# Optimization experiments

Measured on AMD Instinct MI355X. Metric: run time of the kernel, lower is better.

## Reference

```python
import jax, jax.numpy as jnp
import numpy as np
from jax import lax
import math

S, V, D, L, B = 64, 50257, 586, 4, 32  # seq_len, num_tokens, num_inputs, num_layers, batch_size
K1 = S // 4 + 1   # 17, conv1 kernel
P1 = S // 16 + 1  # 5,  avgpool1 kernel
P2 = S // 32 + 1  # 3,  avgpool2 kernel
EPS = 1e-5


def setup_inputs() -> dict:
    key = jax.random.key(0)
    ks = jax.random.split(key, 14)
    tokens = jax.random.randint(ks[0], (S, B), 0, V)
    emb = jax.random.normal(ks[1], (V, D - 3), jnp.float32) * 0.02
    # pos_embeds = randn(S,1,3).repeat(1,B,1)
    pos = jnp.tile(jax.random.normal(ks[2], (S, 1, 3), jnp.float32), (1, B, 1))
    gamma = 1.0 + 0.1 * jax.random.normal(ks[3], (L, S), jnp.float32)
    beta = 0.1 * jax.random.normal(ks[4], (L, S), jnp.float32)
    w1 = jax.random.normal(ks[5], (B // 2, B, K1), jnp.float32) * 0.02
    b1 = jax.random.normal(ks[6], (B // 2,), jnp.float32) * 0.02
    w2 = jax.random.normal(ks[7], (B // 4, B // 2, 1), jnp.float32) * 0.02
    b2 = jax.random.normal(ks[8], (B // 4,), jnp.float32) * 0.02
    w3 = jax.random.normal(ks[9], (B, B // 4, 3), jnp.float32) * 0.02
    b3 = jax.random.normal(ks[10], (B,), jnp.float32) * 0.02
    wl = jax.random.normal(ks[11], (128, 36), jnp.float32) * 0.1
    bl = jax.random.normal(ks[12], (128,), jnp.float32) * 0.1
    return {"tokens": tokens, "emb": emb, "pos": pos, "gamma": gamma, "beta": beta,
            "w1": w1, "b1": b1, "w2": w2, "b2": b2, "w3": w3, "b3": b3,
            "wl": wl, "bl": bl}


def _conv1d(x, w, b):
    # x: (N, C_in, Lx), w: (C_out, C_in, K)
    y = lax.conv_general_dilated(x, w, (1,), 'VALID',
                                 dimension_numbers=('NCH', 'OIH', 'NCH'))
    return y + b[None, :, None]


def _avgpool1d(x, k):
    # torch AvgPool1d: stride=kernel, floor mode
    n, c, lx = x.shape
    lo = lx // k
    return x[:, :, :lo * k].reshape(n, c, lo, k).mean(axis=-1)


def _logits(tokens, emb, pos, gamma, beta, w1, b1, w2, b2, w3, b3, wl, bl):
    x = emb[tokens] * math.sqrt(D)          # (S, B, D-3)
    x = jnp.concatenate([x, pos], axis=2)   # (S, B, D)
    for l in range(L):
        xb = x.swapaxes(0, 1)               # (B, S, D): BatchNorm1d over channels=S
        mean = xb.mean(axis=(0, 2), keepdims=True)
        var = xb.var(axis=(0, 2), keepdims=True)  # biased, training-mode batch stats
        xb = gamma[l][None, :, None] * (xb - mean) * lax.rsqrt(var + EPS) + beta[l][None, :, None]
        x = xb.swapaxes(0, 1)
    out = _conv1d(x, w1, b1)                # (S, B/2, D-16) = (64, 16, 570)
    out = _avgpool1d(out, P1)               # (64, 16, 114)
    out = _conv1d(out, w2, b2)              # (64, 8, 114)
    out = _avgpool1d(out, P2)               # (64, 8, 38)
    out = _conv1d(out, w3, b3)              # (64, 32, 36)
    out = jnp.einsum('sbk,vk->sbv', out, wl) + bl  # (64, 32, 128)
    return out


def reference(tokens, emb, pos, gamma, beta, w1, b1, w2, b2, w3, b3, wl, bl):
    out = _logits(tokens, emb, pos, gamma, beta, w1, b1, w2, b2, w3, b3, wl, bl)
    # vectorized replacement for the triple-nested .item() argmax loop
    return jnp.argmax(out, axis=-1).astype(jnp.float32)  # (S, B)
```

## Files before the change

kernel.cpp:

```cpp
#include <hip/hip_runtime.h>
#include <math.h>

#define SS 64
#define BB 32
#define DD 586
#define DE 583
#define U1 114
#define U2 38
#define T3 36
#define NTOK 18752

__global__ __launch_bounds__(256) void k_stats(
    const int* __restrict__ tokens, const float* __restrict__ emb,
    const float* __restrict__ pos, const float* __restrict__ gamma,
    const float* __restrict__ beta, float* __restrict__ alpha,
    float* __restrict__ delta)
{
  const int s = blockIdx.x;
  const int tid = threadIdx.x;
  const float sqrtD = 24.207436873820409f;
  __shared__ int stok[BB];
  if (tid < BB) stok[tid] = tokens[s*BB + tid];
  __syncthreads();
  double sum = 0.0, sq = 0.0;
  for (int idx = tid; idx < BB*DE; idx += 256) {
    int b = idx / DE;
    int d = idx - b*DE;
    float v = emb[(size_t)stok[b]*DE + d] * sqrtD;
    sum += v; sq += (double)v * v;
  }
  if (tid < BB*3) {
    float v = pos[s*BB*3 + tid];
    sum += v; sq += (double)v * v;
  }
  for (int off = 32; off > 0; off >>= 1) {
    sum += __shfl_down(sum, off);
    sq  += __shfl_down(sq, off);
  }
  __shared__ double rs_[4], rq_[4];
  int wid = tid >> 6;
  if ((tid & 63) == 0) { rs_[wid] = sum; rq_[wid] = sq; }
  __syncthreads();
  if (tid == 0) {
    double St = rs_[0]+rs_[1]+rs_[2]+rs_[3];
    double Qt = rq_[0]+rq_[1]+rq_[2]+rq_[3];
    double m0d = St / (double)NTOK;
    float m0 = (float)m0d;
    float v0 = (float)(Qt / (double)NTOK - m0d*m0d);
    float a = 1.0f;
    for (int l = 0; l < 4; ++l) {
      float rs = 1.0f / sqrtf(a*a*v0 + 1e-5f);
      a = gamma[l*SS + s] * rs * a;
    }
    alpha[s] = a;
    delta[s] = beta[3*SS + s] - a * m0;
  }
}

__global__ __launch_bounds__(256) void k_conv1(
    const int* __restrict__ tokens, const float* __restrict__ emb,
    const float* __restrict__ pos, const float* __restrict__ w1,
    const float* __restrict__ alpha, const float* __restrict__ delta,
    float* __restrict__ part)
{
  const int s = blockIdx.x;
  const int g = blockIdx.y;
  const int tid = threadIdx.x;
  const float sqrtD = 24.207436873820409f;
  __shared__ float xs[8*587];
  __shared__ __align__(16) float wp[8*21*16];
  __shared__ int stok[8];
  if (tid < 8) stok[tid] = tokens[s*BB + g*8 + tid];
  __syncthreads();
  const float al = alpha[s], de = delta[s];
  for (int idx = tid; idx < 8*DD; idx += 256) {
    int cc = idx / DD;
    int d = idx - cc*DD;
    float v;
    if (d < DE) v = emb[(size_t)stok[cc]*DE + d] * sqrtD;
    else        v = pos[(s*BB + g*8 + cc)*3 + (d - DE)];
    xs[cc*587 + d] = al * v + de;
  }
  for (int idx = tid; idx < 8*21*16; idx += 256) {
    int o  = idx & 15;
    int r  = idx >> 4;
    int cc = r / 21;
    int m  = r - cc*21;
    int c  = g*8 + cc;
    int k0 = m - 4; if (k0 < 0) k0 = 0;
    int k1 = m;     if (k1 > 16) k1 = 16;
    float acc = 0.f;
    for (int k = k0; k <= k1; ++k) acc += w1[(o*BB + c)*17 + k];
    wp[idx] = acc * 0.2f;
  }
  __syncthreads();
  const int lane = tid & 63;
  const int og1  = tid >> 6;
  const int u0   = lane;
  const bool u1v = (lane + 64) < U1;
  const int u1   = u1v ? (lane + 64) : (U1 - 1);
  float a00=0,a01=0,a02=0,a03=0, a10=0,a11=0,a12=0,a13=0;
  for (int cc = 0; cc < 8; ++cc) {
    const float* xr = &xs[cc*587];
    const float4* wr = (const float4*)&wp[cc*21*16 + og1*4];
    #pragma unroll
    for (int m = 0; m < 21; ++m) {
      float4 w4 = wr[m*4];
      float x0 = xr[5*u0 + m];
      float x1 = xr[5*u1 + m];
      a00 += x0*w4.x; a01 += x0*w4.y; a02 += x0*w4.z; a03 += x0*w4.w;
      a10 += x1*w4.x; a11 += x1*w4.y; a12 += x1*w4.z; a13 += x1*w4.w;
    }
  }
  float* pb = part + (size_t)(g*SS + s)*16*U1;
  float r0[4] = {a00,a01,a02,a03};
  float r1[4] = {a10,a11,a12,a13};
  #pragma unroll
  for (int oo = 0; oo < 4; ++oo) {
    int o = og1*4 + oo;
    pb[o*U1 + u0] = r0[oo];
    if (u1v) pb[o*U1 + u1] = r1[oo];
  }
}

__global__ __launch_bounds__(256) void k_tail(
    const float* __restrict__ part, const float* __restrict__ b1,
    const float* __restrict__ w2, const float* __restrict__ b2,
    const float* __restrict__ w3, const float* __restrict__ b3,
    const float* __restrict__ wl, const float* __restrict__ bl,
    float* __restrict__ out)
{
  const int s = blockIdx.x;
  const int tid = threadIdx.x;
  __shared__ float o2[16*U1];
  __shared__ float p2[16*U2];
  __shared__ float o4[8*U2];
  __shared__ float o5[32*T3];
  __shared__ float wlb[128*37];
  __shared__ float blb[128];
  for (int idx = tid; idx < 16*U1; idx += 256) {
    int o = idx / U1;
    float acc = b1[o];
    #pragma unroll
    for (int gg = 0; gg < 4; ++gg)
      acc += part[(size_t)(gg*SS + s)*16*U1 + idx];
    o2[idx] = acc;
  }
  for (int idx = tid; idx < 128*36; idx += 256) {
    int v = idx / 36; int t = idx - v*36;
    wlb[v*37 + t] = wl[idx];
  }
  if (tid < 128) blb[tid] = bl[tid];
  __syncthreads();
  for (int idx = tid; idx < 16*U2; idx += 256) {
    int o = idx / U2; int v = idx - o*U2;
    p2[idx] = (o2[o*U1 + 3*v] + o2[o*U1 + 3*v+1] + o2[o*U1 + 3*v+2]) * (1.f/3.f);
  }
  __syncthreads();
  for (int idx = tid; idx < 8*U2; idx += 256) {
    int p = idx / U2; int v = idx - p*U2;
    float acc = b2[p];
    #pragma unroll
    for (int o = 0; o < 16; ++o) acc += p2[o*U2 + v] * w2[p*16 + o];
    o4[idx] = acc;
  }
  __syncthreads();
  for (int idx = tid; idx < 32*T3; idx += 256) {
    int q = idx / T3; int t = idx - q*T3;
    float acc = b3[q];
    #pragma unroll
    for (int p = 0; p < 8; ++p) {
      acc += o4[p*U2 + t    ] * w3[(q*8+p)*3 + 0]
           + o4[p*U2 + t + 1] * w3[(q*8+p)*3 + 1]
           + o4[p*U2 + t + 2] * w3[(q*8+p)*3 + 2];
    }
    o5[idx] = acc;
  }
  __syncthreads();
  const int q = tid >> 3, vs = tid & 7;
  float best = -1e30f; int bidx = 0;
  for (int i = 0; i < 16; ++i) {
    int v = vs + 8*i;
    float acc = blb[v];
    const float* wr = &wlb[v*37];
    const float* orow = &o5[q*T3];
    #pragma unroll
    for (int t = 0; t < 36; ++t) acc += orow[t] * wr[t];
    if (acc > best) { best = acc; bidx = v; }
  }
  #pragma unroll
  for (int off = 1; off < 8; off <<= 1) {
    float ov = __shfl_xor(best, off);
    int oi = __shfl_xor(bidx, off);
    if (ov > best || (ov == best && oi < bidx)) { best = ov; bidx = oi; }
  }
  if (vs == 0) out[s*BB + q] = (float)bidx;
}

extern "C" void kernel_launch(void* const* d_in, const int* in_sizes, int n_in,
                              void* d_out, int out_size, void* d_ws, size_t ws_size,
                              hipStream_t stream)
{
  const int*   tokens = (const int*)  d_in[0];
  const float* emb    = (const float*)d_in[1];
  const float* pos    = (const float*)d_in[2];
  const float* gamma  = (const float*)d_in[3];
  const float* beta   = (const float*)d_in[4];
  const float* w1     = (const float*)d_in[5];
  const float* b1     = (const float*)d_in[6];
  const float* w2     = (const float*)d_in[7];
  const float* b2     = (const float*)d_in[8];
  const float* w3     = (const float*)d_in[9];
  const float* b3     = (const float*)d_in[10];
  const float* wl     = (const float*)d_in[11];
  const float* bl     = (const float*)d_in[12];
  float* out = (float*)d_out;

  float* wsf   = (float*)d_ws;
  float* alpha = wsf;
  float* delta = wsf + 64;
  float* part  = wsf + 128;

  k_stats<<<dim3(SS), dim3(256), 0, stream>>>(tokens, emb, pos, gamma, beta,
                                              alpha, delta);
  k_conv1<<<dim3(SS, 4), dim3(256), 0, stream>>>(tokens, emb, pos, w1,
                                                 alpha, delta, part);
  k_tail<<<dim3(SS), dim3(256), 0, stream>>>(part, b1, w2, b2, w3, b3,
                                             wl, bl, out);
}
```

Baseline: 230.7 us.

## Fuse stats, conv1 and tail into one 512-thread kernel per sequence position

```diff
diff --git a/kernel.cpp b/kernel.cpp
--- a/kernel.cpp
+++ b/kernel.cpp
@@ -9,187 +9,183 @@
 #define U2 38
 #define T3 36
 #define NTOK 18752
-
-__global__ __launch_bounds__(256) void k_stats(
+#define NT 512
+
+__global__ __launch_bounds__(NT) void k_fused(
     const int* __restrict__ tokens, const float* __restrict__ emb,
     const float* __restrict__ pos, const float* __restrict__ gamma,
-    const float* __restrict__ beta, float* __restrict__ alpha,
-    float* __restrict__ delta)
+    const float* __restrict__ beta, const float* __restrict__ w1,
+    const float* __restrict__ b1, const float* __restrict__ w2,
+    const float* __restrict__ b2, const float* __restrict__ w3,
+    const float* __restrict__ b3, const float* __restrict__ wl,
+    const float* __restrict__ bl, float* __restrict__ out)
 {
   const int s = blockIdx.x;
   const int tid = threadIdx.x;
   const float sqrtD = 24.207436873820409f;
+
+  __shared__ union {
+    float xs[8*587];
+    struct {
+      float p2[16*U2];
+      float o4[8*U2];
+      float o5[32*T3];
+    } t;
+  } u;
+  __shared__ __align__(16) float wp[8*21*16];
+  __shared__ float o2[16*U1];
+  __shared__ float wlb[128*37];
+  __shared__ float blb[128];
   __shared__ int stok[BB];
+  __shared__ double rs_[8], rq_[8];
+  __shared__ float sAl, sDe;
+
   if (tid < BB) stok[tid] = tokens[s*BB + tid];
-  __syncthreads();
-  double sum = 0.0, sq = 0.0;
-  for (int idx = tid; idx < BB*DE; idx += 256) {
-    int b = idx / DE;
-    int d = idx - b*DE;
-    float v = emb[(size_t)stok[b]*DE + d] * sqrtD;
-    sum += v; sq += (double)v * v;
+  for (int idx = tid; idx < 128*36; idx += NT) {
+    int v = idx / 36; int t = idx - v*36;
+    wlb[v*37 + t] = wl[idx];
+  }
+  if (tid < 128) blb[tid] = bl[tid];
+  __syncthreads();
+
+  double s0=0.0,s1=0.0,s2=0.0,s3=0.0, q0=0.0,q1=0.0,q2=0.0,q3=0.0;
+  int idx = tid;
+  for (; idx + 3*NT < BB*DE; idx += 4*NT) {
+    int i0=idx, i1=idx+NT, i2=idx+2*NT, i3=idx+3*NT;
+    int b0=i0/DE, b1_=i1/DE, b2_=i2/DE, b3_=i3/DE;
+    float v0 = emb[(size_t)stok[b0]*DE + (i0-b0*DE)] * sqrtD;
+    float v1 = emb[(size_t)stok[b1_]*DE + (i1-b1_*DE)] * sqrtD;
+    float v2 = emb[(size_t)stok[b2_]*DE + (i2-b2_*DE)] * sqrtD;
+    float v3 = emb[(size_t)stok[b3_]*DE + (i3-b3_*DE)] * sqrtD;
+    s0+=v0; q0+=(double)v0*v0; s1+=v1; q1+=(double)v1*v1;
+    s2+=v2; q2+=(double)v2*v2; s3+=v3; q3+=(double)v3*v3;
+  }
+  for (; idx < BB*DE; idx += NT) {
+    int b = idx/DE;
+    float v = emb[(size_t)stok[b]*DE + (idx-b*DE)] * sqrtD;
+    s0+=v; q0+=(double)v*v;
   }
   if (tid < BB*3) {
     float v = pos[s*BB*3 + tid];
-    sum += v; sq += (double)v * v;
-  }
+    s0+=v; q0+=(double)v*v;
+  }
+  double sum = (s0+s1)+(s2+s3);
+  double sq  = (q0+q1)+(q2+q3);
   for (int off = 32; off > 0; off >>= 1) {
     sum += __shfl_down(sum, off);
     sq  += __shfl_down(sq, off);
   }
-  __shared__ double rs_[4], rq_[4];
   int wid = tid >> 6;
   if ((tid & 63) == 0) { rs_[wid] = sum; rq_[wid] = sq; }
   __syncthreads();
   if (tid == 0) {
-    double St = rs_[0]+rs_[1]+rs_[2]+rs_[3];
-    double Qt = rq_[0]+rq_[1]+rq_[2]+rq_[3];
+    double St=0.0, Qt=0.0;
+    for (int w = 0; w < 8; ++w) { St += rs_[w]; Qt += rq_[w]; }
     double m0d = St / (double)NTOK;
     float m0 = (float)m0d;
     float v0 = (float)(Qt / (double)NTOK - m0d*m0d);
     float a = 1.0f;
     for (int l = 0; l < 4; ++l) {
-      float rs = 1.0f / sqrtf(a*a*v0 + 1e-5f);
-      a = gamma[l*SS + s] * rs * a;
-    }
-    alpha[s] = a;
-    delta[s] = beta[3*SS + s] - a * m0;
-  }
-}
-
-__global__ __launch_bounds__(256) void k_conv1(
-    const int* __restrict__ tokens, const float* __restrict__ emb,
-    const float* __restrict__ pos, const float* __restrict__ w1,
-    const float* __restrict__ alpha, const float* __restrict__ delta,
-    float* __restrict__ part)
-{
-  const int s = blockIdx.x;
-  const int g = blockIdx.y;
-  const int tid = threadIdx.x;
-  const float sqrtD = 24.207436873820409f;
-  __shared__ float xs[8*587];
-  __shared__ __align__(16) float wp[8*21*16];
-  __shared__ int stok[8];
-  if (tid < 8) stok[tid] = tokens[s*BB + g*8 + tid];
-  __syncthreads();
-  const float al = alpha[s], de = delta[s];
-  for (int idx = tid; idx < 8*DD; idx += 256) {
-    int cc = idx / DD;
-    int d = idx - cc*DD;
-    float v;
-    if (d < DE) v = emb[(size_t)stok[cc]*DE + d] * sqrtD;
-    else        v = pos[(s*BB + g*8 + cc)*3 + (d - DE)];
-    xs[cc*587 + d] = al * v + de;
-  }
-  for (int idx = tid; idx < 8*21*16; idx += 256) {
-    int o  = idx & 15;
-    int r  = idx >> 4;
-    int cc = r / 21;
-    int m  = r - cc*21;
-    int c  = g*8 + cc;
-    int k0 = m - 4; if (k0 < 0) k0 = 0;
-    int k1 = m;     if (k1 > 16) k1 = 16;
-    float acc = 0.f;
-    for (int k = k0; k <= k1; ++k) acc += w1[(o*BB + c)*17 + k];
-    wp[idx] = acc * 0.2f;
-  }
-  __syncthreads();
+      float r = 1.0f / sqrtf(a*a*v0 + 1e-5f);
+      a = gamma[l*SS + s] * r * a;
+    }
+    sAl = a;
+    sDe = beta[3*SS + s] - a * m0;
+  }
+  __syncthreads();
+  const float al = sAl, de = sDe;
+
   const int lane = tid & 63;
-  const int og1  = tid >> 6;
+  const int og   = tid >> 6;
   const int u0   = lane;
   const bool u1v = (lane + 64) < U1;
   const int u1   = u1v ? (lane + 64) : (U1 - 1);
-  float a00=0,a01=0,a02=0,a03=0, a10=0,a11=0,a12=0,a13=0;
-  for (int cc = 0; cc < 8; ++cc) {
-    const float* xr = &xs[cc*587];
-    const float4* wr = (const float4*)&wp[cc*21*16 + og1*4];
-    #pragma unroll
-    for (int m = 0; m < 21; ++m) {
-      float4 w4 = wr[m*4];
-      float x0 = xr[5*u0 + m];
-      float x1 = xr[5*u1 + m];
-      a00 += x0*w4.x; a01 += x0*w4.y; a02 += x0*w4.z; a03 += x0*w4.w;
-      a10 += x1*w4.x; a11 += x1*w4.y; a12 += x1*w4.z; a13 += x1*w4.w;
-    }
-  }
-  float* pb = part + (size_t)(g*SS + s)*16*U1;
-  float r0[4] = {a00,a01,a02,a03};
-  float r1[4] = {a10,a11,a12,a13};
-  #pragma unroll
-  for (int oo = 0; oo < 4; ++oo) {
-    int o = og1*4 + oo;
-    pb[o*U1 + u0] = r0[oo];
-    if (u1v) pb[o*U1 + u1] = r1[oo];
-  }
-}
-
-__global__ __launch_bounds__(256) void k_tail(
-    const float* __restrict__ part, const float* __restrict__ b1,
-    const float* __restrict__ w2, const float* __restrict__ b2,
-    const float* __restrict__ w3, const float* __restrict__ b3,
-    const float* __restrict__ wl, const float* __restrict__ bl,
-    float* __restrict__ out)
-{
-  const int s = blockIdx.x;
-  const int tid = threadIdx.x;
-  __shared__ float o2[16*U1];
-  __shared__ float p2[16*U2];
-  __shared__ float o4[8*U2];
-  __shared__ float o5[32*T3];
-  __shared__ float wlb[128*37];
-  __shared__ float blb[128];
-  for (int idx = tid; idx < 16*U1; idx += 256) {
-    int o = idx / U1;
-    float acc = b1[o];
-    #pragma unroll
-    for (int gg = 0; gg < 4; ++gg)
-      acc += part[(size_t)(gg*SS + s)*16*U1 + idx];
-    o2[idx] = acc;
-  }
-  for (int idx = tid; idx < 128*36; idx += 256) {
-    int v = idx / 36; int t = idx - v*36;
-    wlb[v*37 + t] = wl[idx];
-  }
-  if (tid < 128) blb[tid] = bl[tid];
-  __syncthreads();
-  for (int idx = tid; idx < 16*U2; idx += 256) {
-    int o = idx / U2; int v = idx - o*U2;
-    p2[idx] = (o2[o*U1 + 3*v] + o2[o*U1 + 3*v+1] + o2[o*U1 + 3*v+2]) * (1.f/3.f);
-  }
-  __syncthreads();
-  for (int idx = tid; idx < 8*U2; idx += 256) {
-    int p = idx / U2; int v = idx - p*U2;
+  float a00=0.f, a01=0.f, a10=0.f, a11=0.f;
+  for (int g = 0; g < 4; ++g) {
+    __syncthreads();
+    for (int i = tid; i < 8*DD; i += NT) {
+      int cc = i / DD;
+      int d = i - cc*DD;
+      float v;
+      if (d < DE) v = emb[(size_t)stok[g*8+cc]*DE + d] * sqrtD;
+      else        v = pos[(s*BB + g*8 + cc)*3 + (d - DE)];
+      u.xs[cc*587 + d] = al * v + de;
+    }
+    for (int i = tid; i < 8*21*16; i += NT) {
+      int o  = i & 15;
+      int r  = i >> 4;
+      int cc = r / 21;
+      int m  = r - cc*21;
+      int c  = g*8 + cc;
+      int k0 = m - 4;  if (k0 < 0) k0 = 0;
+      int k1 = m;      if (k1 > 16) k1 = 16;
+      float acc = 0.f;
+      for (int k = k0; k <= k1; ++k) acc += w1[(o*BB + c)*17 + k];
+      wp[i] = acc * 0.2f;
+    }
+    __syncthreads();
+    for (int cc = 0; cc < 8; ++cc) {
+      const float* xr = &u.xs[cc*587];
+      const float2* wr = (const float2*)&wp[cc*21*16 + og*2];
+      #pragma unroll
+      for (int m = 0; m < 21; ++m) {
+        float2 w2v = wr[m*8];
+        float x0 = xr[5*u0 + m];
+        float x1 = xr[5*u1 + m];
+        a00 += x0*w2v.x; a01 += x0*w2v.y;
+        a10 += x1*w2v.x; a11 += x1*w2v.y;
+      }
+    }
+  }
+  {
+    int o0 = og*2, o1 = og*2 + 1;
+    o2[o0*U1 + u0] = a00 + b1[o0];
+    o2[o1*U1 + u0] = a01 + b1[o1];
+    if (u1v) {
+      o2[o0*U1 + u1] = a10 + b1[o0];
+      o2[o1*U1 + u1] = a11 + b1[o1];
+    }
+  }
+  __syncthreads();
+
+  for (int i2 = tid; i2 < 16*U2; i2 += NT) {
+    int o = i2 / U2; int v = i2 - o*U2;
+    u.t.p2[i2] = (o2[o*U1 + 3*v] + o2[o*U1 + 3*v+1] + o2[o*U1 + 3*v+2]) * (1.f/3.f);
+  }
+  __syncthreads();
+  for (int i2 = tid; i2 < 8*U2; i2 += NT) {
+    int p = i2 / U2; int v = i2 - p*U2;
     float acc = b2[p];
     #pragma unroll
-    for (int o = 0; o < 16; ++o) acc += p2[o*U2 + v] * w2[p*16 + o];
-    o4[idx] = acc;
-  }
-  __syncthreads();
-  for (int idx = tid; idx < 32*T3; idx += 256) {
-    int q = idx / T3; int t = idx - q*T3;
+    for (int o = 0; o < 16; ++o) acc += u.t.p2[o*U2 + v] * w2[p*16 + o];
+    u.t.o4[i2] = acc;
+  }
+  __syncthreads();
+  for (int i2 = tid; i2 < 32*T3; i2 += NT) {
+    int q = i2 / T3; int t = i2 - q*T3;
     float acc = b3[q];
     #pragma unroll
     for (int p = 0; p < 8; ++p) {
-      acc += o4[p*U2 + t    ] * w3[(q*8+p)*3 + 0]
-           + o4[p*U2 + t + 1] * w3[(q*8+p)*3 + 1]
-           + o4[p*U2 + t + 2] * w3[(q*8+p)*3 + 2];
-    }
-    o5[idx] = acc;
-  }
-  __syncthreads();
-  const int q = tid >> 3, vs = tid & 7;
+      acc += u.t.o4[p*U2 + t    ] * w3[(q*8+p)*3 + 0]
+           + u.t.o4[p*U2 + t + 1] * w3[(q*8+p)*3 + 1]
+           + u.t.o4[p*U2 + t + 2] * w3[(q*8+p)*3 + 2];
+    }
+    u.t.o5[i2] = acc;
+  }
+  __syncthreads();
+  const int q = tid >> 4, vs = tid & 15;
   float best = -1e30f; int bidx = 0;
-  for (int i = 0; i < 16; ++i) {
-    int v = vs + 8*i;
+  const float* orow = &u.t.o5[q*T3];
+  for (int i = 0; i < 8; ++i) {
+    int v = vs + 16*i;
     float acc = blb[v];
     const float* wr = &wlb[v*37];
-    const float* orow = &o5[q*T3];
     #pragma unroll
     for (int t = 0; t < 36; ++t) acc += orow[t] * wr[t];
     if (acc > best) { best = acc; bidx = v; }
   }
   #pragma unroll
-  for (int off = 1; off < 8; off <<= 1) {
+  for (int off = 1; off < 16; off <<= 1) {
     float ov = __shfl_xor(best, off);
     int oi = __shfl_xor(bidx, off);
     if (ov > best || (ov == best && oi < bidx)) { best = ov; bidx = oi; }
@@ -216,15 +212,7 @@
   const float* bl     = (const float*)d_in[12];
   float* out = (float*)d_out;
 
-  float* wsf   = (float*)d_ws;
-  float* alpha = wsf;
-  float* delta = wsf + 64;
-  float* part  = wsf + 128;
-
-  k_stats<<<dim3(SS), dim3(256), 0, stream>>>(tokens, emb, pos, gamma, beta,
-                                              alpha, delta);
-  k_conv1<<<dim3(SS, 4), dim3(256), 0, stream>>>(tokens, emb, pos, w1,
-                                                 alpha, delta, part);
-  k_tail<<<dim3(SS), dim3(256), 0, stream>>>(part, b1, w2, b2, w3, b3,
-                                             wl, bl, out);
+  k_fused<<<dim3(SS), dim3(NT), 0, stream>>>(tokens, emb, pos, gamma, beta,
+                                             w1, b1, w2, b2, w3, b3, wl, bl,
+                                             out);
 }
```

Result: no change. 230.5 us (-0.1%).

## Split stats into per-row blocks and precompute pooled conv weights once

Applied to the files above, without the earlier changes.

```diff
diff --git a/kernel.cpp b/kernel.cpp
--- a/kernel.cpp
+++ b/kernel.cpp
@@ -9,117 +9,118 @@
 #define U2 38
 #define T3 36
 #define NTOK 18752
-
-__global__ __launch_bounds__(256) void k_stats(
-    const int* __restrict__ tokens, const float* __restrict__ emb,
-    const float* __restrict__ pos, const float* __restrict__ gamma,
-    const float* __restrict__ beta, float* __restrict__ alpha,
-    float* __restrict__ delta)
-{
-  const int s = blockIdx.x;
-  const int tid = threadIdx.x;
-  const float sqrtD = 24.207436873820409f;
-  __shared__ int stok[BB];
-  if (tid < BB) stok[tid] = tokens[s*BB + tid];
-  __syncthreads();
-  double sum = 0.0, sq = 0.0;
-  for (int idx = tid; idx < BB*DE; idx += 256) {
-    int b = idx / DE;
-    int d = idx - b*DE;
-    float v = emb[(size_t)stok[b]*DE + d] * sqrtD;
-    sum += v; sq += (double)v * v;
-  }
-  if (tid < BB*3) {
-    float v = pos[s*BB*3 + tid];
-    sum += v; sq += (double)v * v;
-  }
-  for (int off = 32; off > 0; off >>= 1) {
-    sum += __shfl_down(sum, off);
-    sq  += __shfl_down(sq, off);
-  }
-  __shared__ double rs_[4], rq_[4];
-  int wid = tid >> 6;
-  if ((tid & 63) == 0) { rs_[wid] = sum; rq_[wid] = sq; }
-  __syncthreads();
-  if (tid == 0) {
-    double St = rs_[0]+rs_[1]+rs_[2]+rs_[3];
-    double Qt = rq_[0]+rq_[1]+rq_[2]+rq_[3];
-    double m0d = St / (double)NTOK;
-    float m0 = (float)m0d;
-    float v0 = (float)(Qt / (double)NTOK - m0d*m0d);
-    float a = 1.0f;
-    for (int l = 0; l < 4; ++l) {
-      float rs = 1.0f / sqrtf(a*a*v0 + 1e-5f);
-      a = gamma[l*SS + s] * rs * a;
-    }
-    alpha[s] = a;
-    delta[s] = beta[3*SS + s] - a * m0;
-  }
-}
-
-__global__ __launch_bounds__(256) void k_conv1(
+#define NSTAT (SS*BB)
+#define WPN (32*21*16)
+#define WPBLK (WPN/256)
+#define SQD 24.207436873820409f
+
+
+__global__ __launch_bounds__(256) void k_pre(
     const int* __restrict__ tokens, const float* __restrict__ emb,
     const float* __restrict__ pos, const float* __restrict__ w1,
-    const float* __restrict__ alpha, const float* __restrict__ delta,
-    float* __restrict__ part)
-{
-  const int s = blockIdx.x;
-  const int g = blockIdx.y;
-  const int tid = threadIdx.x;
-  const float sqrtD = 24.207436873820409f;
-  __shared__ float xs[8*587];
-  __shared__ __align__(16) float wp[8*21*16];
-  __shared__ int stok[8];
-  if (tid < 8) stok[tid] = tokens[s*BB + g*8 + tid];
-  __syncthreads();
-  const float al = alpha[s], de = delta[s];
-  for (int idx = tid; idx < 8*DD; idx += 256) {
-    int cc = idx / DD;
-    int d = idx - cc*DD;
-    float v;
-    if (d < DE) v = emb[(size_t)stok[cc]*DE + d] * sqrtD;
-    else        v = pos[(s*BB + g*8 + cc)*3 + (d - DE)];
-    xs[cc*587 + d] = al * v + de;
-  }
-  for (int idx = tid; idx < 8*21*16; idx += 256) {
-    int o  = idx & 15;
-    int r  = idx >> 4;
-    int cc = r / 21;
-    int m  = r - cc*21;
-    int c  = g*8 + cc;
-    int k0 = m - 4; if (k0 < 0) k0 = 0;
-    int k1 = m;     if (k1 > 16) k1 = 16;
+    double* __restrict__ rowsumd, double* __restrict__ rowsqd,
+    float* __restrict__ wp)
+{
+  const int bid = blockIdx.x, tid = threadIdx.x;
+  if (bid < NSTAT) {
+    const int s = bid >> 5, b = bid & 31;
+    const int tok = tokens[s*BB + b];
+    const float* row = emb + (size_t)tok*DE;
+    double sum = 0.0, sq = 0.0;
+    for (int d = tid; d < DE; d += 256) {
+      float v = row[d] * SQD;
+      sum += v; sq += (double)v*v;
+    }
+    if (tid < 3) {
+      float v = pos[(s*BB + b)*3 + tid];
+      sum += v; sq += (double)v*v;
+    }
+    for (int off = 32; off > 0; off >>= 1) {
+      sum += __shfl_down(sum, off);
+      sq  += __shfl_down(sq, off);
+    }
+    __shared__ double rs[4], rq[4];
+    if ((tid & 63) == 0) { rs[tid>>6] = sum; rq[tid>>6] = sq; }
+    __syncthreads();
+    if (tid == 0) {
+      rowsumd[bid] = (rs[0]+rs[1]) + (rs[2]+rs[3]);
+      rowsqd[bid]  = (rq[0]+rq[1]) + (rq[2]+rq[3]);
+    }
+  } else {
+    const int idx = (bid - NSTAT)*256 + tid;
+    const int o = idx & 15;
+    const int r = idx >> 4;
+    const int m = r % 21;
+    const int c = r / 21;
+    int k0 = m - 4;  if (k0 < 0)  k0 = 0;
+    int k1 = m;      if (k1 > 16) k1 = 16;
     float acc = 0.f;
     for (int k = k0; k <= k1; ++k) acc += w1[(o*BB + c)*17 + k];
     wp[idx] = acc * 0.2f;
   }
-  __syncthreads();
-  const int lane = tid & 63;
-  const int og1  = tid >> 6;
-  const int u0   = lane;
-  const bool u1v = (lane + 64) < U1;
-  const int u1   = u1v ? (lane + 64) : (U1 - 1);
-  float a00=0,a01=0,a02=0,a03=0, a10=0,a11=0,a12=0,a13=0;
+}
+
+__global__ __launch_bounds__(256) void k_conv(
+    const int* __restrict__ tokens, const float* __restrict__ emb,
+    const float* __restrict__ pos, const float* __restrict__ wp,
+    const double* __restrict__ rowsumd, const double* __restrict__ rowsqd,
+    const float* __restrict__ gamma, const float* __restrict__ beta,
+    float* __restrict__ part)
+{
+  const int s = blockIdx.x, g = blockIdx.y;
+  const int tid = threadIdx.x;
+  __shared__ float xs[8*DD];
+  __shared__ int stok[8];
+  __shared__ float sAl, sDe;
+  if (tid < 8) stok[tid] = tokens[s*BB + g*8 + tid];
+  __syncthreads();
+  for (int i = tid; i < 8*DD; i += 256) {
+    int cc = i / DD, d = i - cc*DD;
+    float v = (d < DE) ? emb[(size_t)stok[cc]*DE + d] * SQD
+                       : pos[(s*BB + g*8 + cc)*3 + (d - DE)];
+    xs[i] = v;
+  }
+  if (tid < 32) {
+    double sm = rowsumd[s*BB + tid], qq = rowsqd[s*BB + tid];
+    for (int off = 16; off > 0; off >>= 1) {
+      sm += __shfl_down(sm, off, 32);
+      qq += __shfl_down(qq, off, 32);
+    }
+    if (tid == 0) {
+      double m0d = sm / (double)NTOK;
+      float m0 = (float)m0d;
+      float v0 = (float)(qq / (double)NTOK - m0d*m0d);
+      float a = 1.0f;
+      for (int l = 0; l < 4; ++l) {
+        float r = 1.0f / sqrtf(a*a*v0 + 1e-5f);
+        a = gamma[l*SS + s] * r * a;
+      }
+      sAl = a;
+      sDe = beta[3*SS + s] - a*m0;
+    }
+  }
+  __syncthreads();
+  const float al = sAl, de = sDe;
+  const int up = tid & 127;
+  const int oh = __builtin_amdgcn_readfirstlane(tid >> 7);
+  const int u  = (up < U1) ? up : (U1 - 1);
+  float acc[8] = {0,0,0,0,0,0,0,0};
   for (int cc = 0; cc < 8; ++cc) {
-    const float* xr = &xs[cc*587];
-    const float4* wr = (const float4*)&wp[cc*21*16 + og1*4];
+    const float* xr = &xs[cc*DD + 5*u];
+    float xv[21];
+    #pragma unroll
+    for (int m = 0; m < 21; ++m) { float v = xr[m]; xv[m] = al * v + de; }
+    const float* wr = wp + ((g*8 + cc)*21)*16 + oh*8;
     #pragma unroll
     for (int m = 0; m < 21; ++m) {
-      float4 w4 = wr[m*4];
-      float x0 = xr[5*u0 + m];
-      float x1 = xr[5*u1 + m];
-      a00 += x0*w4.x; a01 += x0*w4.y; a02 += x0*w4.z; a03 += x0*w4.w;
-      a10 += x1*w4.x; a11 += x1*w4.y; a12 += x1*w4.z; a13 += x1*w4.w;
-    }
-  }
-  float* pb = part + (size_t)(g*SS + s)*16*U1;
-  float r0[4] = {a00,a01,a02,a03};
-  float r1[4] = {a10,a11,a12,a13};
-  #pragma unroll
-  for (int oo = 0; oo < 4; ++oo) {
-    int o = og1*4 + oo;
-    pb[o*U1 + u0] = r0[oo];
-    if (u1v) pb[o*U1 + u1] = r1[oo];
+      #pragma unroll
+      for (int j = 0; j < 8; ++j) acc[j] += xv[m] * wr[m*16 + j];
+    }
+  }
+  if (up < U1) {
+    float* pb = part + ((size_t)(g*SS + s)*16 + oh*8)*U1 + up;
+    #pragma unroll
+    for (int j = 0; j < 8; ++j) pb[j*U1] = acc[j];
   }
 }
 
@@ -130,43 +131,43 @@
     const float* __restrict__ wl, const float* __restrict__ bl,
     float* __restrict__ out)
 {
-  const int s = blockIdx.x;
-  const int tid = threadIdx.x;
+  const int s = blockIdx.x, tid = threadIdx.x;
   __shared__ float o2[16*U1];
   __shared__ float p2[16*U2];
   __shared__ float o4[8*U2];
   __shared__ float o5[32*T3];
   __shared__ float wlb[128*37];
   __shared__ float blb[128];
+  for (int idx = tid; idx < 128*36; idx += 256) {
+    int v = idx / 36, t = idx - v*36;
+    wlb[v*37 + t] = wl[idx];
+  }
+  if (tid < 128) blb[tid] = bl[tid];
   for (int idx = tid; idx < 16*U1; idx += 256) {
     int o = idx / U1;
     float acc = b1[o];
-    #pragma unroll
-    for (int gg = 0; gg < 4; ++gg)
-      acc += part[(size_t)(gg*SS + s)*16*U1 + idx];
+    acc += part[(size_t)(0*SS + s)*16*U1 + idx];
+    acc += part[(size_t)(1*SS + s)*16*U1 + idx];
+    acc += part[(size_t)(2*SS + s)*16*U1 + idx];
+    acc += part[(size_t)(3*SS + s)*16*U1 + idx];
     o2[idx] = acc;
   }
-  for (int idx = tid; idx < 128*36; idx += 256) {
-    int v = idx / 36; int t = idx - v*36;
-    wlb[v*37 + t] = wl[idx];
-  }
-  if (tid < 128) blb[tid] = bl[tid];
-  __syncthreads();
-  for (int idx = tid; idx < 16*U2; idx += 256) {
-    int o = idx / U2; int v = idx - o*U2;
-    p2[idx] = (o2[o*U1 + 3*v] + o2[o*U1 + 3*v+1] + o2[o*U1 + 3*v+2]) * (1.f/3.f);
-  }
-  __syncthreads();
-  for (int idx = tid; idx < 8*U2; idx += 256) {
-    int p = idx / U2; int v = idx - p*U2;
+  __syncthreads();
+  for (int i2 = tid; i2 < 16*U2; i2 += 256) {
+    int o = i2 / U2, v = i2 - o*U2;
+    p2[i2] = (o2[o*U1 + 3*v] + o2[o*U1 + 3*v+1] + o2[o*U1 + 3*v+2]) * (1.f/3.f);
+  }
+  __syncthreads();
+  for (int i2 = tid; i2 < 8*U2; i2 += 256) {
+    int p = i2 / U2, v = i2 - p*U2;
     float acc = b2[p];
     #pragma unroll
     for (int o = 0; o < 16; ++o) acc += p2[o*U2 + v] * w2[p*16 + o];
-    o4[idx] = acc;
-  }
-  __syncthreads();
-  for (int idx = tid; idx < 32*T3; idx += 256) {
-    int q = idx / T3; int t = idx - q*T3;
+    o4[i2] = acc;
+  }
+  __syncthreads();
+  for (int i2 = tid; i2 < 32*T3; i2 += 256) {
+    int q = i2 / T3, t = i2 - q*T3;
     float acc = b3[q];
     #pragma unroll
     for (int p = 0; p < 8; ++p) {
@@ -174,16 +175,16 @@
            + o4[p*U2 + t + 1] * w3[(q*8+p)*3 + 1]
            + o4[p*U2 + t + 2] * w3[(q*8+p)*3 + 2];
     }
-    o5[idx] = acc;
+    o5[i2] = acc;
   }
   __syncthreads();
   const int q = tid >> 3, vs = tid & 7;
   float best = -1e30f; int bidx = 0;
+  const float* orow = &o5[q*T3];
   for (int i = 0; i < 16; ++i) {
     int v = vs + 8*i;
     float acc = blb[v];
     const float* wr = &wlb[v*37];
-    const float* orow = &o5[q*T3];
     #pragma unroll
     for (int t = 0; t < 36; ++t) acc += orow[t] * wr[t];
     if (acc > best) { best = acc; bidx = v; }
@@ -216,15 +217,15 @@
   const float* bl     = (const float*)d_in[12];
   float* out = (float*)d_out;
 
-  float* wsf   = (float*)d_ws;
-  float* alpha = wsf;
-  float* delta = wsf + 64;
-  float* part  = wsf + 128;
-
-  k_stats<<<dim3(SS), dim3(256), 0, stream>>>(tokens, emb, pos, gamma, beta,
-                                              alpha, delta);
-  k_conv1<<<dim3(SS, 4), dim3(256), 0, stream>>>(tokens, emb, pos, w1,
-                                                 alpha, delta, part);
+  double* rowsumd = (double*)d_ws;
+  double* rowsqd  = rowsumd + NSTAT;
+  float*  wp      = (float*)(rowsqd + NSTAT);
+  float*  part    = wp + WPN;
+
+  k_pre<<<dim3(NSTAT + WPBLK), dim3(256), 0, stream>>>(
+      tokens, emb, pos, w1, rowsumd, rowsqd, wp);
+  k_conv<<<dim3(SS, 4), dim3(256), 0, stream>>>(
+      tokens, emb, pos, wp, rowsumd, rowsqd, gamma, beta, part);
   k_tail<<<dim3(SS), dim3(256), 0, stream>>>(part, b1, w2, b2, w3, b3,
                                              wl, bl, out);
 }
```

Result: faster. 201.6 us (-12.6%).
